# Optimization experiments

Hardware: AMD Instinct MI355X
Metric: run time of the kernel (lower is better)

## Reference

```python
import jax, jax.numpy as jnp
import numpy as np

L, B, D, H = 128, 4, 768, 300
NT, NR = 7, 12  # ner tags, relation types
EPS = 1e-5


def _cummax(v):
    # torch: cumsum(softmax(v, -1), -1)
    return jnp.cumsum(jax.nn.softmax(v, axis=-1), axis=-1)


def _layernorm(v, g, b):
    mu = jnp.mean(v, axis=-1, keepdims=True)
    var = jnp.var(v, axis=-1, keepdims=True)
    return (v - mu) * jax.lax.rsqrt(var + EPS) * g + b


def setup_inputs() -> dict:
    key = jax.random.key(0)
    ks = jax.random.split(key, 24)
    s = lambda fan_in: 1.0 / np.sqrt(fan_in)
    u = lambda k, shape, sc: jax.random.uniform(k, shape, jnp.float32, -sc, sc)
    inp = {
        "x": jax.random.normal(ks[0], (L, B, D), jnp.float32),
        "mask": jnp.ones((L, B), jnp.float32),
        # PFN_Unit
        "W_ih": u(ks[1], (5 * H, D), s(D)), "b_ih": u(ks[2], (5 * H,), s(D)),
        "W_hh": u(ks[3], (5 * H, H), s(H)), "b_hh": u(ks[4], (5 * H,), s(H)),
        "W_tr": u(ks[5], (H, 3 * H), s(3 * H)), "b_tr": u(ks[6], (H,), s(3 * H)),
        # NERUnit
        "n_W": u(ks[7], (H, 2 * H), s(2 * H)), "n_b": u(ks[8], (H,), s(2 * H)),
        "ner_hW": u(ks[9], (H, 3 * H), s(3 * H)), "ner_hb": u(ks[10], (H,), s(3 * H)),
        "ner_g": jnp.ones((H,), jnp.float32), "ner_beta": jnp.zeros((H,), jnp.float32),
        "ner_tW": u(ks[11], (NT, H), s(H)), "ner_tb": u(ks[12], (NT,), s(H)),
        # ReUnit
        "r_W": u(ks[13], (H, 2 * H), s(2 * H)), "r_b": u(ks[14], (H,), s(2 * H)),
        "re_hW": u(ks[15], (H, 3 * H), s(3 * H)), "re_hb": u(ks[16], (H,), s(3 * H)),
        "re_g": jnp.ones((H,), jnp.float32), "re_beta": jnp.zeros((H,), jnp.float32),
        "re_tW": u(ks[17], (NR, H), s(H)), "re_tb": u(ks[18], (NR,), s(H)),
    }
    return inp


def _encoder(x, W_ih, b_ih, W_hh, b_hh, W_tr, b_tr):
    pre = jnp.einsum('lbd,gd->lbg', x, W_ih) + b_ih  # precompute input transform [L,B,5H]

    def step(carry, gx):
        h, c_in = carry
        gates = gx + h @ W_hh.T + b_hh
        c, eg_cin, rg_cin, eg_c, rg_c = jnp.split(gates, 5, axis=1)
        eg_cin, rg_cin = 1.0 - _cummax(eg_cin), _cummax(rg_cin)
        eg_c, rg_c = 1.0 - _cummax(eg_c), _cummax(rg_c)
        c = jnp.tanh(c)
        ov_c = rg_c * eg_c
        up_c, dn_c = rg_c - ov_c, eg_c - ov_c
        ov_i = rg_cin * eg_cin
        up_i, dn_i = rg_cin - ov_i, eg_cin - ov_i
        share = ov_i * c_in + ov_c * c
        c_re = up_i * c_in + up_c * c + share
        c_ner = dn_i * c_in + dn_c * c + share
        c_out = jnp.concatenate([c_re, c_ner, share], axis=-1) @ W_tr.T + b_tr
        h_out = jnp.tanh(c_out)
        return (h_out, c_out), (jnp.tanh(c_ner), jnp.tanh(c_re), jnp.tanh(share))

    h0 = jnp.zeros((x.shape[1], W_hh.shape[1]), x.dtype)
    _, (h_ner, h_re, h_share) = jax.lax.scan(step, (h0, h0), pre)
    return h_ner, h_re, h_share  # each [L,B,H]


def _pair_unit(h_task, h_share, mask, gW, gb, hW, hb, ln_g, ln_b, tW, tb, diag):
    length = h_task.shape[0]
    # global feature: tanh(Linear(cat(share, task))), max over time
    h_glob = jnp.tanh(jnp.concatenate([h_share, h_task], axis=-1) @ gW.T + gb)  # [L,B,H]
    g = jnp.max(h_glob, axis=0)  # [B,H]
    # pairwise feature [L,L,B,3H] = cat(start, end, global)
    st = jnp.broadcast_to(h_task[:, None], (length, length) + h_task.shape[1:])
    en = jnp.broadcast_to(h_task[None, :], (length, length) + h_task.shape[1:])
    gb4 = jnp.broadcast_to(g, (length, length) + g.shape)
    feat = jnp.concatenate([st, en, gb4], axis=-1)
    out = _layernorm(feat @ hW.T + hb, ln_g, ln_b)
    out = jax.nn.elu(out)  # eval mode: dropout is identity
    out = jax.nn.sigmoid(out @ tW.T + tb)  # [L,L,B,T]
    # mask
    m = mask[:, None, :] * mask[None, :, :]  # [L,L,B]
    if diag:
        m = m * jnp.triu(jnp.ones((length, length), out.dtype))[:, :, None]
    return out * m[..., None]


def reference(x, mask, W_ih, b_ih, W_hh, b_hh, W_tr, b_tr,
              n_W, n_b, ner_hW, ner_hb, ner_g, ner_beta, ner_tW, ner_tb,
              r_W, r_b, re_hW, re_hb, re_g, re_beta, re_tW, re_tb):
    h_ner, h_re, h_share = _encoder(x, W_ih, b_ih, W_hh, b_hh, W_tr, b_tr)
    ner = _pair_unit(h_ner, h_share, mask, n_W, n_b, ner_hW, ner_hb,
                     ner_g, ner_beta, ner_tW, ner_tb, diag=True)
    re = _pair_unit(h_re, h_share, mask, r_W, r_b, re_hW, re_hb,
                    re_g, re_beta, re_tW, re_tb, diag=False)
    return ner, re
```

## Files before the change

### kernel.cpp

```cpp
#include <hip/hip_runtime.h>

#define LLEN 128
#define BB 4
#define DD 768
#define HH 300
#define G5 1500
#define H3 900
#define NTT 7
#define NRR 12
#define NCHB 10
#define RPB 150
#define OPB 30

#define C_WIH  0
#define C_X    1152000
#define C_WHH2 1545216
#define C_WTR2 1995216
#define F_BIH  2265216
#define F_BTR  2266720
#define F_PRE  2267040
#define F_HG0  (F_PRE)
#define F_HG1  (F_PRE+153600)
#define F_A0   (F_PRE+307200)
#define F_E0   (F_PRE+460800)
#define F_GF0  (F_PRE+616832)
#define F_GF1  (F_PRE+618048)
#define F_HNER (F_PRE+768000)
#define F_HRE  (F_HNER+153600)
#define F_HSH  (F_HRE+153600)
#define F_A1   0
#define F_E1   153600
#define F_AUX  (F_HSH+153600)
#define AUXB   2432
#define AUX_FL 9728
#define WS_NEED_BYTES ((size_t)(F_AUX+11776)*4)

typedef unsigned short u16;
typedef unsigned int u32;
typedef float f4 __attribute__((ext_vector_type(4)));

__device__ __forceinline__ float bf2f(u16 u) {
  union { u32 i; float f; } v; v.i = ((u32)u) << 16; return v.f;
}
__device__ __forceinline__ u16 f2bf(float f) {
  union { float f; u32 i; } v; v.f = f;
  u32 r = v.i + 0x7fffu + ((v.i >> 16) & 1u);
  return (u16)(r >> 16);
}
__device__ __forceinline__ float ldin(const void* p, int i, bool f32) {
  return f32 ? ((const float*)p)[i] : bf2f(((const u16*)p)[i]);
}
__device__ __forceinline__ bool is32(const void* mk) {
  return ((const u16*)mk)[0] == 0;
}
__device__ __forceinline__ float wsum(float x) {
  #pragma unroll
  for (int d = 1; d < 64; d <<= 1) x += __shfl_xor(x, d);
  return x;
}
__device__ __forceinline__ float aload(const float* p) {
  int v = __hip_atomic_load((const int*)p, __ATOMIC_RELAXED, __HIP_MEMORY_SCOPE_AGENT);
  union { int i; float f; } u; u.i = v; return u.f;
}
__device__ __forceinline__ void astore(float* p, float v) {
  union { float f; int i; } u; u.f = v;
  __hip_atomic_store((int*)p, u.i, __ATOMIC_RELAXED, __HIP_MEMORY_SCOPE_AGENT);
}
__device__ __forceinline__ void gbar(int* flag, int tid, int target) {
  __syncthreads();
  if (tid == 0) {
    __builtin_amdgcn_s_waitcnt(0);
    __hip_atomic_fetch_add(flag, 1, __ATOMIC_RELAXED, __HIP_MEMORY_SCOPE_AGENT);
    while (__hip_atomic_load(flag, __ATOMIC_RELAXED, __HIP_MEMORY_SCOPE_AGENT) < target)
      __builtin_amdgcn_s_sleep(1);
  }
  __syncthreads();
}

__device__ __forceinline__ f4 ld4_l2(const f4* p) {
  f4 v;
  asm volatile("global_load_dwordx4 %0, %1, off sc0\n\ts_waitcnt vmcnt(0)"
               : "=v"(v) : "v"(p) : "memory");
  return v;
}
__device__ __forceinline__ float ld1_l2(const float* p) {
  float v;
  asm volatile("global_load_dword %0, %1, off sc0\n\ts_waitcnt vmcnt(0)"
               : "=v"(v) : "v"(p) : "memory");
  return v;
}
__device__ __forceinline__ int ldi_l2(const int* p) {
  int v;
  asm volatile("global_load_dword %0, %1, off sc0\n\ts_waitcnt vmcnt(0)"
               : "=v"(v) : "v"(p) : "memory");
  return v;
}
__device__ __forceinline__ void gbarL2(int* flag, int tid, int target) {
  __builtin_amdgcn_s_waitcnt(0);
  __syncthreads();
  if (tid == 0) {
    __builtin_amdgcn_s_waitcnt(0);
    __hip_atomic_fetch_add(flag, 1, __ATOMIC_RELAXED, __HIP_MEMORY_SCOPE_WORKGROUP);
    int it = 0;
    while (ldi_l2(flag) < target) {
      __builtin_amdgcn_s_sleep(1);
      if (++it > 100000) break;
    }
  }
  __syncthreads();
}
__device__ __forceinline__ void exst(float* p, float v, int mode) {
  if (mode) *p = v; else astore(p, v);
}

__global__ void k_canon(const void* xo, const void* mk, const void* Wih, const void* bih,
                        const void* Whh, const void* bhh, const void* Wtr, const void* btr,
                        float* ws) {
  bool f32 = is32(mk);
  int piece = blockIdx.y;
  int i = blockIdx.x * 256 + threadIdx.x;
  switch (piece) {
    case 0: if (!f32 && i < 1152000) ws[C_WIH + i] = ldin(Wih, i, f32); break;
    case 1: if (!f32 && i < 393216)  ws[C_X + i]   = ldin(xo, i, f32);  break;
    case 2: if (i < 225000) {
      int k2 = i / G5, out = i - k2 * G5;
      float2 v;
      v.x = ldin(Whh, out * HH + 2 * k2, f32);
      v.y = ldin(Whh, out * HH + 2 * k2 + 1, f32);
      ((float2*)(ws + C_WHH2))[i] = v;
    } break;
    case 3: if (i < 135000) {
      int k2 = i / HH, out = i - k2 * HH;
      float2 v;
      v.x = ldin(Wtr, out * H3 + 2 * k2, f32);
      v.y = ldin(Wtr, out * H3 + 2 * k2 + 1, f32);
      ((float2*)(ws + C_WTR2))[i] = v;
    } break;
    case 4: {
      if (i < 1504) ws[F_BIH + i] = (i < G5) ? ldin(bih, i, f32) + ldin(bhh, i, f32) : 0.f;
      else if (i < 1824) { int j = i - 1504; ws[F_BTR + j] = (j < HH) ? ldin(btr, j, f32) : 0.f; }
    } break;
    case 5: if (i < 11776) ws[F_AUX + i] = 0.f; break;
  }
}

__global__ void k_pre2(const void* xo, const void* Wo, const void* mk,
                       const float* cX, const float* cW, const float* biasf, float* pre) {
  bool f32 = is32(mk);
  const float* X = f32 ? (const float*)xo : cX;
  const float* W = f32 ? (const float*)Wo : cW;
  __shared__ __align__(16) float xl[8 * DD];
  int tid = threadIdx.x;
  int lb0 = (blockIdx.x >> 1) * 8;
  int half = blockIdx.x & 1;
  for (int e = tid; e < 8 * DD; e += 256) xl[e] = X[(size_t)lb0 * DD + e];
  __syncthreads();
  for (int j = half * 750 + tid; j < half * 750 + 750; j += 256) {
    const float4* w = (const float4*)(W + (size_t)j * DD);
    float acc[8] = {0.f, 0.f, 0.f, 0.f, 0.f, 0.f, 0.f, 0.f};
    #pragma unroll 2
    for (int k = 0; k < DD / 4; ++k) {
      float4 u = w[k];
      #pragma unroll
      for (int r = 0; r < 8; ++r) {
        const float4 p = *(const float4*)(xl + r * DD + k * 4);
        acc[r] += u.x * p.x + u.y * p.y + u.z * p.z + u.w * p.w;
      }
    }
    float bias = biasf[j];
    #pragma unroll
    for (int r = 0; r < 8; ++r) pre[(size_t)(lb0 + r) * G5 + j] = acc[r] + bias;
  }
}

__global__ void __launch_bounds__(512, 2) k_scan6(const float* pre, const float2* W2h, const float2* W2t,
                                                  const float* btrf, float* hner, float* hre, float* hsh,
                                                  float* aux) {
  __shared__ __align__(16) float h_l[304];
  __shared__ __align__(16) float ci_l[304];
  __shared__ __align__(16) float ga_l[1504];
  __shared__ __align__(16) float cat_l[904];
  __shared__ __align__(16) float ps[512];
  __shared__ __align__(16) float sums_l[8];
  __shared__ float exv[160];
  __shared__ float pp[40];
  __shared__ int s_bc;
  __shared__ int s_mode;
  int tid = threadIdx.x;
  int* ibase = (int*)(aux + AUX_FL);
  if (tid == 0) {
    int* cl = ibase + 1024;
    unsigned xcd;
    asm volatile("s_getreg_b32 %0, hwreg(HW_REG_XCC_ID)" : "=s"(xcd));
    xcd &= 7u;
    int rank = __hip_atomic_fetch_add(cl + xcd, 1, __ATOMIC_RELAXED, __HIP_MEMORY_SCOPE_AGENT);
    __hip_atomic_fetch_add(cl + 8, 1, __ATOMIC_RELAXED, __HIP_MEMORY_SCOPE_AGENT);
    int it = 0;
    while (__hip_atomic_load(cl + 8, __ATOMIC_RELAXED, __HIP_MEMORY_SCOPE_AGENT) < (int)gridDim.x) {
      __builtin_amdgcn_s_sleep(2);
      if (++it > 200000) break;
    }
    int base = 0;
    for (unsigned x = 0; x < xcd; ++x)
      base += __hip_atomic_load(cl + x, __ATOMIC_RELAXED, __HIP_MEMORY_SCOPE_AGENT) / NCHB;
    int cnt = __hip_atomic_load(cl + xcd, __ATOMIC_RELAXED, __HIP_MEMORY_SCOPE_AGENT);
    int slot = base + rank / NCHB;
    s_bc = (rank < (cnt / NCHB) * NCHB && slot < BB) ? (slot * 16 + rank % NCHB) : -1;
  }
  __syncthreads();
  int bc = s_bc;
  if (bc < 0) return;
  int b = bc >> 4, ch = bc & 15;
  int s = ch >> 1;
  int r0 = ch * RPB;
  float* gb   = aux + b * AUXB;
  float* cb   = gb + 1504;
  float* hb   = gb + 1808;
  float* sums = gb + 2112;
  int* flags = ibase + b * 256;

  {
    int* atf = ibase + 1088 + b * 32;
    float* tst = gb + 2176;
    int* seflag = (int*)(gb + 2208);
    if (ch == 0 && tid == 0) tst[0] = 1.0f;
    gbar(atf + 0, tid, NCHB);
    if (tid == 0) { float w1 = ld1_l2(tst); (void)w1; }
    gbar(atf + 1, tid, NCHB);
    if (ch == 0 && tid == 0) {
      tst[0] = 2.0f;
      __builtin_amdgcn_s_waitcnt(0);
    }
    if (ch == 1 && tid == 0)
      __hip_atomic_fetch_add(seflag, 1, __ATOMIC_RELAXED, __HIP_MEMORY_SCOPE_WORKGROUP);
    gbar(atf + 2, tid, NCHB);
    if (tid == 0) {
      float w2 = ld1_l2(tst);
      int fv = ldi_l2(seflag);
      if (w2 != 2.0f || fv != 1)
        __hip_atomic_fetch_or(atf + 4, 1, __ATOMIC_RELAXED, __HIP_MEMORY_SCOPE_AGENT);
    }
    gbar(atf + 3, tid, NCHB);
    if (tid == 0)
      s_mode = (__hip_atomic_load(atf + 4, __ATOMIC_RELAXED, __HIP_MEMORY_SCOPE_AGENT) == 0) ? 1 : 0;
    __syncthreads();
  }
  int mode = s_mode;

  for (int i = tid; i < 304; i += 512) { h_l[i] = 0.f; ci_l[i] = 0.f; }
  int j = tid / RPB, r = tid - j * RPB;
  int o2 = tid % OPB, jj = tid / OPB;
  int kb = j * 100;

  float2 wh[50];
  if (tid < 450) {
    const float2* wp = W2h + (size_t)(j * 50) * G5 + (r0 + r);
    #pragma unroll
    for (int kk = 0; kk < 50; ++kk) wh[kk] = wp[(size_t)kk * G5];
  }
  float2 wt[29];
  int k2b = jj * 29;
  int k2e = (k2b + 29 < 450) ? (k2b + 29) : 450;
  int nk2 = k2e - k2b;
  if (tid < 480) {
    const float2* wp = W2t + (size_t)k2b * HH + (ch * OPB + o2);
    #pragma unroll
    for (int q = 0; q < 29; ++q) if (q < nk2) wt[q] = wp[(size_t)q * HH];
  }
  __syncthreads();

  for (int t = 0; t < LLEN; ++t) {
    float pv = 0.f;
    if (j == 0 && tid < 450) pv = pre[((size_t)t * BB + b) * G5 + r0 + r];
    if (t > 0) {
      if (mode) {
        if (tid < 75)       { f4 v = ld4_l2((const f4*)hb + tid); *(f4*)(h_l + 4 * tid) = v; }
        else if (tid < 150) { int q = tid - 75; f4 v = ld4_l2((const f4*)cb + q); *(f4*)(ci_l + 4 * q) = v; }
      } else {
        for (int i = tid; i < HH; i += 512) { h_l[i] = aload(hb + i); ci_l[i] = aload(cb + i); }
      }
      __syncthreads();
    }
    if (tid < 450) {
      float acc = pv;
      if (t > 0) {
        #pragma unroll
        for (int kk = 0; kk < 50; ++kk)
          acc += wh[kk].x * h_l[kb + 2 * kk] + wh[kk].y * h_l[kb + 2 * kk + 1];
      }
      ps[tid] = acc;
    }
    __syncthreads();
    if (tid < RPB) {
      float g = ps[tid] + ps[RPB + tid] + ps[2 * RPB + tid];
      if (s == 0) exst(gb + r0 + tid, tanhf(g), mode);
      else exv[tid] = __expf(g);
    }
    __syncthreads();
    if (s > 0) {
      if (tid < 30) {
        int base2 = tid * 5;
        pp[tid] = ((exv[base2] + exv[base2+1]) + (exv[base2+2] + exv[base2+3])) + exv[base2+4];
      }
      __syncthreads();
      if (tid == 0) {
        float run = 0.f;
        for (int i = 0; i < 30; ++i) { float tv = pp[i]; pp[i] = run; run += tv; }
        exst(sums + (ch - 2), run, mode);
      }
      __syncthreads();
      if (tid < 30) {
        int base2 = tid * 5;
        float run = pp[tid];
        run += exv[base2];     exst(gb + r0 + base2,     run, mode);
        run += exv[base2 + 1]; exst(gb + r0 + base2 + 1, run, mode);
        run += exv[base2 + 2]; exst(gb + r0 + base2 + 2, run, mode);
        run += exv[base2 + 3]; exst(gb + r0 + base2 + 3, run, mode);
        run += exv[base2 + 4]; exst(gb + r0 + base2 + 4, run, mode);
      }
    }
    if (mode) gbarL2(flags + 2 * t, tid, NCHB); else gbar(flags + 2 * t, tid, NCHB);
    if (mode) {
      if (tid < 375)      { f4 v = ld4_l2((const f4*)gb + tid); *(f4*)(ga_l + 4 * tid) = v; }
      else if (tid < 377) { int q = tid - 375; f4 v = ld4_l2((const f4*)sums + q); *(f4*)(sums_l + 4 * q) = v; }
    } else {
      for (int i = tid; i < G5; i += 512) ga_l[i] = aload(gb + i);
      if (tid < 8) sums_l[tid] = aload(sums + tid);
    }
    __syncthreads();
    if (tid < HH) {
      float c = ga_l[tid];
      float v[4];
      #pragma unroll
      for (int s1 = 0; s1 < 4; ++s1) {
        float raw = ga_l[(s1 + 1) * HH + tid];
        float off = (tid >= RPB) ? sums_l[2 * s1] : 0.f;
        float S = sums_l[2 * s1] + sums_l[2 * s1 + 1];
        v[s1] = (raw + off) / S;
      }
      float eg_cin = 1.f - v[0], rg_cin = v[1], eg_c = 1.f - v[2], rg_c = v[3];
      float ci = (t > 0) ? ci_l[tid] : 0.f;
      float ov_c = rg_c * eg_c;
      float up_c = rg_c - ov_c, dn_c = eg_c - ov_c;
      float ov_i = rg_cin * eg_cin;
      float up_i = rg_cin - ov_i, dn_i = eg_cin - ov_i;
      float share = ov_i * ci + ov_c * c;
      float c_re  = up_i * ci + up_c * c + share;
      float c_ner = dn_i * ci + dn_c * c + share;
      cat_l[tid] = c_re; cat_l[HH + tid] = c_ner; cat_l[2 * HH + tid] = share;
      int sb = ch * OPB;
      if (tid >= sb && tid < sb + OPB) {
        size_t ob = ((size_t)t * BB + b) * HH + tid;
        hner[ob] = tanhf(c_ner); hre[ob] = tanhf(c_re); hsh[ob] = tanhf(share);
      }
    }
    __syncthreads();
    if (tid < 480) {
      float acc = 0.f;
      #pragma unroll
      for (int q = 0; q < 29; ++q)
        if (q < nk2) acc += wt[q].x * cat_l[2 * (k2b + q)] + wt[q].y * cat_l[2 * (k2b + q) + 1];
      ps[tid] = acc;
    }
    __syncthreads();
    if (tid < OPB) {
      float co = btrf[ch * OPB + tid];
      #pragma unroll
      for (int q = 0; q < 16; ++q) co += ps[q * OPB + tid];
      exst(cb + ch * OPB + tid, co, mode);
      exst(hb + ch * OPB + tid, tanhf(co), mode);
    }
    if (mode) gbarL2(flags + 2 * t + 1, tid, NCHB); else gbar(flags + 2 * t + 1, tid, NCHB);
  }
}

__global__ void k_glob3(const float* hsh, const float* hner, const float* hre,
                        const void* nW, const void* nb, const void* rW, const void* rb,
                        const void* mk, float* hg0, float* hg1) {
  bool f32 = is32(mk);
  int task = blockIdx.x >> 7;
  int lb0 = (blockIdx.x & 127) * 4;
  const float* tsk = task ? hre : hner;
  const void* gWo = task ? rW : nW;
  const void* gbo = task ? rb : nb;
  float* hg = task ? hg1 : hg0;
  __shared__ __align__(16) float catl[2400];
  int tid = threadIdx.x;
  for (int e = tid; e < 2400; e += 320) {
    int rr = e / 600, c = e - rr * 600;
    catl[e] = (c < HH) ? hsh[(size_t)(lb0 + rr) * HH + c] : tsk[(size_t)(lb0 + rr) * HH + (c - HH)];
  }
  __syncthreads();
  if (tid < HH) {
    float bias = ldin(gbo, tid, f32);
    float acc[4] = {bias, bias, bias, bias};
    if (f32) {
      const float4* row = (const float4*)((const float*)gWo + (size_t)tid * 600);
      #pragma unroll 2
      for (int k = 0; k < 150; ++k) {
        float4 u = row[k];
        #pragma unroll
        for (int rr = 0; rr < 4; ++rr) {
          const float4 cv = *(const float4*)(catl + rr * 600 + 4 * k);
          acc[rr] += u.x * cv.x + u.y * cv.y + u.z * cv.z + u.w * cv.w;
        }
      }
    } else {
      for (int k = 0; k < 600; ++k) {
        float w = ldin(gWo, tid * 600 + k, f32);
        #pragma unroll
        for (int rr = 0; rr < 4; ++rr) acc[rr] += w * catl[rr * 600 + k];
      }
    }
    #pragma unroll
    for (int rr = 0; rr < 4; ++rr) hg[(size_t)(lb0 + rr) * HH + tid] = tanhf(acc[rr]);
  }
}

__global__ void k_feat2(const float* hner, const float* hre,
                        const void* nhW, const void* nhb, const void* rhW, const void* rhb,
                        const void* mk, float* A0, float* E0, float* A1, float* E1) {
  bool f32 = is32(mk);
  int task = blockIdx.x >> 7;
  int lb0 = (blockIdx.x & 127) * 4;
  const float* tsk = task ? hre : hner;
  const void* hWo = task ? rhW : nhW;
  const void* hbo = task ? rhb : nhb;
  float* A = task ? A1 : A0;
  float* E = task ? E1 : E0;
  __shared__ __align__(16) float tl[1200];
  int tid = threadIdx.x;
  for (int e = tid; e < 1200; e += 320) {
    int rr = e / 300, c = e - rr * 300;
    tl[e] = tsk[(size_t)(lb0 + rr) * HH + c];
  }
  __syncthreads();
  if (tid < HH) {
    float bias = ldin(hbo, tid, f32);
    float a[4] = {bias, bias, bias, bias};
    float ev[4] = {0.f, 0.f, 0.f, 0.f};
    if (f32) {
      const float4* r1 = (const float4*)((const float*)hWo + (size_t)tid * H3);
      const float4* r2 = (const float4*)((const float*)hWo + (size_t)tid * H3 + HH);
      #pragma unroll 2
      for (int k = 0; k < 75; ++k) {
        float4 u = r1[k], w2 = r2[k];
        #pragma unroll
        for (int rr = 0; rr < 4; ++rr) {
          const float4 tv = *(const float4*)(tl + rr * 300 + 4 * k);
          a[rr]  += u.x * tv.x + u.y * tv.y + u.z * tv.z + u.w * tv.w;
          ev[rr] += w2.x * tv.x + w2.y * tv.y + w2.z * tv.z + w2.w * tv.w;
        }
      }
    } else {
      for (int k = 0; k < HH; ++k) {
        float w1 = ldin(hWo, tid * H3 + k, f32);
        float w2 = ldin(hWo, tid * H3 + HH + k, f32);
        #pragma unroll
        for (int rr = 0; rr < 4; ++rr) {
          a[rr] += w1 * tl[rr * 300 + k];
          ev[rr] += w2 * tl[rr * 300 + k];
        }
      }
    }
    #pragma unroll
    for (int rr = 0; rr < 4; ++rr) {
      A[(size_t)(lb0 + rr) * HH + tid] = a[rr];
      E[(size_t)(lb0 + rr) * HH + tid] = ev[rr];
    }
  }
}

__global__ void k_gmf(const float* hg0, const float* hg1, const void* nhW, const void* rhW,
                      const void* mk, float* Gf0, float* Gf1) {
  bool f32 = is32(mk);
  int task = blockIdx.x >> 2, b = blockIdx.x & 3;
  const float* hg = task ? hg1 : hg0;
  const void* hWo = task ? rhW : nhW;
  float* Gf = task ? Gf1 : Gf0;
  __shared__ __align__(16) float gl[304];
  int tid = threadIdx.x;
  if (tid < HH) {
    float m = -1e30f;
    for (int l = 0; l < LLEN; ++l) m = fmaxf(m, hg[((size_t)l * BB + b) * HH + tid]);
    gl[tid] = m;
  }
  __syncthreads();
  if (tid < HH) {
    float acc = 0.f;
    if (f32) {
      const float4* row = (const float4*)((const float*)hWo + (size_t)tid * H3 + 600);
      #pragma unroll 5
      for (int k = 0; k < 75; ++k) {
        float4 u = row[k];
        const float4 gv = *(const float4*)(gl + 4 * k);
        acc += u.x * gv.x + u.y * gv.y + u.z * gv.z + u.w * gv.w;
      }
    } else {
      for (int k = 0; k < HH; ++k) acc += gl[k] * ldin(hWo, tid * H3 + 600 + k, f32);
    }
    Gf[b * HH + tid] = acc;
  }
}

__global__ void __launch_bounds__(256) k_pair6(const float* A0, const float* E0, const float* Gf0,
                                               const void* lg0, const void* lb0_, const void* tW0, const void* tb0,
                                               const float* A1, const float* E1, const float* Gf1,
                                               const void* lg1, const void* lb1_, const void* tW1, const void* tb1,
                                               const void* mk, void* outv) {
  __shared__ float lg_l[304], lb_l[304], tb_l[16];
  __shared__ float tw_l[3616];
  bool f32 = is32(mk);
  int tau = blockIdx.x >> 12;
  int bid = blockIdx.x & 4095;
  const float* A  = tau ? A1 : A0;
  const float* E  = tau ? E1 : E0;
  const float* Gf = tau ? Gf1 : Gf0;
  const void* lgo = tau ? lg1 : lg0;
  const void* lbo = tau ? lb1_ : lb0_;
  const void* tWo = tau ? tW1 : tW0;
  const void* tbo = tau ? tb1 : tb0;
  int T = tau ? NRR : NTT;
  int diag = tau ? 0 : 1;
  int Toff = tau ? 458752 : 0;
  int tid = threadIdx.x;
  for (int i2 = tid; i2 < HH; i2 += 256) { lg_l[i2] = ldin(lgo, i2, f32); lb_l[i2] = ldin(lbo, i2, f32); }
  for (int i2 = tid; i2 < T * HH; i2 += 256) tw_l[i2] = ldin(tWo, i2, f32);
  if (tid < T) tb_l[tid] = ldin(tbo, tid, f32);
  __syncthreads();
  int i = bid >> 5;
  int j0 = (bid & 31) << 2;
  int b = tid >> 6, ln = tid & 63;
  const float* ar = A  + (size_t)(i * BB + b) * HH;
  const float* gr = Gf + (size_t)b * HH;
  bool ok4 = ln < 44;
  float a0 = ar[ln]       + gr[ln];
  float a1 = ar[64 + ln]  + gr[64 + ln];
  float a2 = ar[128 + ln] + gr[128 + ln];
  float a3 = ar[192 + ln] + gr[192 + ln];
  float a4 = ok4 ? (ar[256 + ln] + gr[256 + ln]) : 0.f;
  float mi = ldin(mk, i * BB + b, f32);
  for (int dj = 0; dj < 4; ++dj) {
    int jx = j0 + dj;
    const float* er = E + (size_t)(jx * BB + b) * HH;
    float u0 = a0 + er[ln];
    float u1 = a1 + er[64 + ln];
    float u2 = a2 + er[128 + ln];
    float u3 = a3 + er[192 + ln];
    float u4 = ok4 ? (a4 + er[256 + ln]) : 0.f;
    float s1 = ((u0 + u1) + (u2 + u3)) + u4;
    float s2 = ((u0 * u0 + u1 * u1) + (u2 * u2 + u3 * u3)) + u4 * u4;
    #pragma unroll
    for (int d = 1; d < 64; d <<= 1) { s1 += __shfl_xor(s1, d); s2 += __shfl_xor(s2, d); }
    float mean = s1 * (1.f / 300.f);
    float var = s2 * (1.f / 300.f) - mean * mean;
    float rstd = rsqrtf(var + 1e-5f);
    {
      float y;
      y = (u0 - mean) * rstd * lg_l[ln]       + lb_l[ln];       u0 = (y > 0.f) ? y : __expf(y) - 1.f;
      y = (u1 - mean) * rstd * lg_l[64 + ln]  + lb_l[64 + ln];  u1 = (y > 0.f) ? y : __expf(y) - 1.f;
      y = (u2 - mean) * rstd * lg_l[128 + ln] + lb_l[128 + ln]; u2 = (y > 0.f) ? y : __expf(y) - 1.f;
      y = (u3 - mean) * rstd * lg_l[192 + ln] + lb_l[192 + ln]; u3 = (y > 0.f) ? y : __expf(y) - 1.f;
      if (ok4) {
        y = (u4 - mean) * rstd * lg_l[256 + ln] + lb_l[256 + ln];
        u4 = (y > 0.f) ? y : __expf(y) - 1.f;
      }
    }
    float m = mi * ldin(mk, jx * BB + b, f32);
    if (diag && jx < i) m = 0.f;
    size_t obase = (size_t)Toff + ((size_t)(i * LLEN + jx) * BB + b) * T;
    float mine = 0.f;
    for (int t = 0; t < T; ++t) {
      const float* twr = tw_l + t * HH;
      float s = u0 * twr[ln] + u1 * twr[64 + ln] + u2 * twr[128 + ln] + u3 * twr[192 + ln];
      if (ok4) s += u4 * twr[256 + ln];
      s = wsum(s);
      s += tb_l[t];
      float o = m / (1.f + __expf(-s));
      mine = (ln == t) ? o : mine;
    }
    if (ln < T) {
      if (f32) ((float*)outv)[obase + ln] = mine;
      else ((u16*)outv)[obase + ln] = f2bf(mine);
    }
  }
}

__global__ void k_sent(const void* mk, const void* xo, void* outv, int hostcode) {
  __shared__ int bad;
  if (threadIdx.x == 0) bad = 0;
  __syncthreads();
  bool f32 = is32(mk);
  for (int i = threadIdx.x; i < 4096; i += 256) {
    float v = ldin(xo, i, f32);
    if (!(v == v) || fabsf(v) > 1e6f) bad = 1;
  }
  __syncthreads();
  if (threadIdx.x == 0) {
    float code = (float)hostcode;
    if (bad) code = fmaxf(code, 88.f);
    if (code > 0.f) {
      if (f32) ((float*)outv)[0] = code;
      else ((u16*)outv)[0] = f2bf(code);
    }
  }
}

extern "C" void kernel_launch(void* const* d_in, const int* in_sizes, int n_in,
                              void* d_out, int out_size, void* d_ws, size_t ws_size,
                              hipStream_t stream) {
  const void* x    = d_in[0];
  const void* mask = d_in[1];
  const void* Wih  = d_in[2];
  const void* bih  = d_in[3];
  const void* Whh  = d_in[4];
  const void* bhh  = d_in[5];
  const void* Wtr  = d_in[6];
  const void* btr  = d_in[7];
  const void* nW   = d_in[8];
  const void* nb   = d_in[9];
  const void* nhW  = d_in[10];
  const void* nhb  = d_in[11];
  const void* ng   = d_in[12];
  const void* nbe  = d_in[13];
  const void* ntW  = d_in[14];
  const void* ntb  = d_in[15];
  const void* rW   = d_in[16];
  const void* rb   = d_in[17];
  const void* rhW  = d_in[18];
  const void* rhb  = d_in[19];
  const void* rg   = d_in[20];
  const void* rbe  = d_in[21];
  const void* rtW  = d_in[22];
  const void* rtb  = d_in[23];
  float* ws = (float*)d_ws;

  static const int exp_sz[24] = {393216, 512, 1152000, 1500, 450000, 1500, 270000, 300,
                                 180000, 300, 270000, 300, 300, 300, 2100, 7,
                                 180000, 300, 270000, 300, 300, 300, 3600, 12};
  int hostcode = 0;
  if (n_in != 24) hostcode = 890;
  else {
    for (int ii = 0; ii < 24; ++ii)
      if (in_sizes[ii] != exp_sz[ii]) { hostcode = 900 + ii; break; }
  }
  if (hostcode == 0 && out_size != 1245184) hostcode = 880;
  if (hostcode == 0 && ws_size < WS_NEED_BYTES) hostcode = 1099;

  dim3 gc(4500, 6);
  k_canon<<<gc, 256, 0, stream>>>(x, mask, Wih, bih, Whh, bhh, Wtr, btr, ws);
  k_pre2<<<128, 256, 0, stream>>>(x, Wih, mask, ws + C_X, ws + C_WIH, ws + F_BIH, ws + F_PRE);
  k_scan6<<<256, 512, 0, stream>>>(ws + F_PRE, (const float2*)(ws + C_WHH2), (const float2*)(ws + C_WTR2),
                                   ws + F_BTR, ws + F_HNER, ws + F_HRE, ws + F_HSH, ws + F_AUX);
  k_glob3<<<256, 320, 0, stream>>>(ws + F_HSH, ws + F_HNER, ws + F_HRE,
                                   nW, nb, rW, rb, mask, ws + F_HG0, ws + F_HG1);
  k_feat2<<<256, 320, 0, stream>>>(ws + F_HNER, ws + F_HRE, nhW, nhb, rhW, rhb, mask,
                                   ws + F_A0, ws + F_E0, ws + F_A1, ws + F_E1);
  k_gmf<<<8, 320, 0, stream>>>(ws + F_HG0, ws + F_HG1, nhW, rhW, mask, ws + F_GF0, ws + F_GF1);
  k_pair6<<<8192, 256, 0, stream>>>(ws + F_A0, ws + F_E0, ws + F_GF0, ng, nbe, ntW, ntb,
                                    ws + F_A1, ws + F_E1, ws + F_GF1, rg, rbe, rtW, rtb,
                                    mask, d_out);
  k_sent<<<1, 256, 0, stream>>>(mask, x, d_out, hostcode);
}
```

Before: 1.527 ms.

## Replace counter barriers with per-chunk slot barriers and prefetch next-step inputs

The recurrent scan kernel's per-step grid barriers, which used an atomic counter per step, are replaced by per-chunk token slots. Each block writes its own slot and 64 threads poll all ten slots with vector loads that bypass the cache. The softmax-cumsum prefix over 30 partial sums becomes a wavefront shuffle scan instead of a serial single-thread loop, which removes two block syncs. The next step's precomputed input is prefetched during the barrier wait, and the final barrier is skipped. Spin timeouts are shortened, which risks silent desync if a block stalls longer than the limit.

```diff
diff --git a/kernel.cpp b/kernel.cpp
--- a/kernel.cpp
+++ b/kernel.cpp
@@ -38,6 +38,7 @@
 typedef unsigned short u16;
 typedef unsigned int u32;
 typedef float f4 __attribute__((ext_vector_type(4)));
+typedef int i4 __attribute__((ext_vector_type(4)));
 
 __device__ __forceinline__ float bf2f(u16 u) {
   union { u32 i; float f; } v; v.i = ((u32)u) << 16; return v.f;
@@ -58,10 +59,6 @@
   for (int d = 1; d < 64; d <<= 1) x += __shfl_xor(x, d);
   return x;
 }
-__device__ __forceinline__ float aload(const float* p) {
-  int v = __hip_atomic_load((const int*)p, __ATOMIC_RELAXED, __HIP_MEMORY_SCOPE_AGENT);
-  union { int i; float f; } u; u.i = v; return u.f;
-}
 __device__ __forceinline__ void astore(float* p, float v) {
   union { float f; int i; } u; u.f = v;
   __hip_atomic_store((int*)p, u.i, __ATOMIC_RELAXED, __HIP_MEMORY_SCOPE_AGENT);
@@ -71,46 +68,100 @@
   if (tid == 0) {
     __builtin_amdgcn_s_waitcnt(0);
     __hip_atomic_fetch_add(flag, 1, __ATOMIC_RELAXED, __HIP_MEMORY_SCOPE_AGENT);
-    while (__hip_atomic_load(flag, __ATOMIC_RELAXED, __HIP_MEMORY_SCOPE_AGENT) < target)
+    int it = 0;
+    while (__hip_atomic_load(flag, __ATOMIC_RELAXED, __HIP_MEMORY_SCOPE_AGENT) < target) {
       __builtin_amdgcn_s_sleep(1);
-  }
-  __syncthreads();
-}
-
-__device__ __forceinline__ f4 ld4_l2(const f4* p) {
+      if (++it > 50000) break;
+    }
+  }
+  __syncthreads();
+}
+__device__ __forceinline__ f4 ld4x(const f4* p, int mode) {
   f4 v;
-  asm volatile("global_load_dwordx4 %0, %1, off sc0\n\ts_waitcnt vmcnt(0)"
-               : "=v"(v) : "v"(p) : "memory");
+  if (mode)
+    asm volatile("global_load_dwordx4 %0, %1, off sc0\n\ts_waitcnt vmcnt(0)"
+                 : "=v"(v) : "v"(p) : "memory");
+  else
+    asm volatile("global_load_dwordx4 %0, %1, off sc0 sc1\n\ts_waitcnt vmcnt(0)"
+                 : "=v"(v) : "v"(p) : "memory");
   return v;
 }
-__device__ __forceinline__ float ld1_l2(const float* p) {
+__device__ __forceinline__ float ld1x(const float* p, int mode) {
   float v;
-  asm volatile("global_load_dword %0, %1, off sc0\n\ts_waitcnt vmcnt(0)"
-               : "=v"(v) : "v"(p) : "memory");
+  if (mode)
+    asm volatile("global_load_dword %0, %1, off sc0\n\ts_waitcnt vmcnt(0)"
+                 : "=v"(v) : "v"(p) : "memory");
+  else
+    asm volatile("global_load_dword %0, %1, off sc0 sc1\n\ts_waitcnt vmcnt(0)"
+                 : "=v"(v) : "v"(p) : "memory");
   return v;
 }
-__device__ __forceinline__ int ldi_l2(const int* p) {
+__device__ __forceinline__ int ldix(const int* p, int mode) {
   int v;
-  asm volatile("global_load_dword %0, %1, off sc0\n\ts_waitcnt vmcnt(0)"
-               : "=v"(v) : "v"(p) : "memory");
+  if (mode)
+    asm volatile("global_load_dword %0, %1, off sc0\n\ts_waitcnt vmcnt(0)"
+                 : "=v"(v) : "v"(p) : "memory");
+  else
+    asm volatile("global_load_dword %0, %1, off sc0 sc1\n\ts_waitcnt vmcnt(0)"
+                 : "=v"(v) : "v"(p) : "memory");
   return v;
-}
-__device__ __forceinline__ void gbarL2(int* flag, int tid, int target) {
-  __builtin_amdgcn_s_waitcnt(0);
-  __syncthreads();
-  if (tid == 0) {
-    __builtin_amdgcn_s_waitcnt(0);
-    __hip_atomic_fetch_add(flag, 1, __ATOMIC_RELAXED, __HIP_MEMORY_SCOPE_WORKGROUP);
-    int it = 0;
-    while (ldi_l2(flag) < target) {
-      __builtin_amdgcn_s_sleep(1);
-      if (++it > 100000) break;
-    }
-  }
-  __syncthreads();
 }
 __device__ __forceinline__ void exst(float* p, float v, int mode) {
   if (mode) *p = v; else astore(p, v);
+}
+__device__ __forceinline__ int poll10(const int* slots, int tok, int mode) {
+  i4 a, b, c;
+  if (mode)
+    asm volatile("global_load_dwordx4 %0, %3, off sc0\n\t"
+                 "global_load_dwordx4 %1, %4, off sc0\n\t"
+                 "global_load_dwordx4 %2, %5, off sc0\n\t"
+                 "s_waitcnt vmcnt(0)"
+                 : "=&v"(a), "=&v"(b), "=&v"(c)
+                 : "v"(slots), "v"(slots + 4), "v"(slots + 8) : "memory");
+  else
+    asm volatile("global_load_dwordx4 %0, %3, off sc0 sc1\n\t"
+                 "global_load_dwordx4 %1, %4, off sc0 sc1\n\t"
+                 "global_load_dwordx4 %2, %5, off sc0 sc1\n\t"
+                 "s_waitcnt vmcnt(0)"
+                 : "=&v"(a), "=&v"(b), "=&v"(c)
+                 : "v"(slots), "v"(slots + 4), "v"(slots + 8) : "memory");
+  return (a.x >= tok) & (a.y >= tok) & (a.z >= tok) & (a.w >= tok) &
+         (b.x >= tok) & (b.y >= tok) & (b.z >= tok) & (b.w >= tok) &
+         (c.x >= tok) & (c.y >= tok);
+}
+__device__ __forceinline__ void sbar(int* slots, int ch, int tok, int tid, int mode) {
+  asm volatile("s_waitcnt vmcnt(0)" ::: "memory");
+  __syncthreads();
+  if (tid == 0) {
+    if (mode) slots[ch] = tok;
+    else __hip_atomic_store(slots + ch, tok, __ATOMIC_RELAXED, __HIP_MEMORY_SCOPE_AGENT);
+  }
+  if (tid < 64) {
+    int it = 0;
+    while (!poll10(slots, tok, mode)) {
+      __builtin_amdgcn_s_sleep(1);
+      if (++it > 5000) break;
+    }
+  }
+  __syncthreads();
+}
+__device__ __forceinline__ int claim_bc(int* cl, int nb) {
+  unsigned xcd;
+  asm volatile("s_getreg_b32 %0, hwreg(HW_REG_XCC_ID)" : "=s"(xcd));
+  xcd &= 7u;
+  int rank = __hip_atomic_fetch_add(cl + xcd, 1, __ATOMIC_RELAXED, __HIP_MEMORY_SCOPE_AGENT);
+  __hip_atomic_fetch_add(cl + 8, 1, __ATOMIC_RELAXED, __HIP_MEMORY_SCOPE_AGENT);
+  int it = 0;
+  while (__hip_atomic_load(cl + 8, __ATOMIC_RELAXED, __HIP_MEMORY_SCOPE_AGENT) < nb) {
+    __builtin_amdgcn_s_sleep(2);
+    if (++it > 100000) break;
+  }
+  int base = 0;
+  for (unsigned x = 0; x < xcd; ++x)
+    base += __hip_atomic_load(cl + x, __ATOMIC_RELAXED, __HIP_MEMORY_SCOPE_AGENT) / NCHB;
+  int cnt = __hip_atomic_load(cl + xcd, __ATOMIC_RELAXED, __HIP_MEMORY_SCOPE_AGENT);
+  int slot = base + rank / NCHB;
+  return (rank < (cnt / NCHB) * NCHB && slot < BB) ? (slot * 16 + rank % NCHB) : -1;
 }
 
 __global__ void k_canon(const void* xo, const void* mk, const void* Wih, const void* bih,
@@ -173,7 +224,7 @@
   }
 }
 
-__global__ void __launch_bounds__(512, 2) k_scan6(const float* pre, const float2* W2h, const float2* W2t,
+__global__ void __launch_bounds__(512, 2) k_scan8(const float* pre, const float2* W2h, const float2* W2t,
                                                   const float* btrf, float* hner, float* hre, float* hsh,
                                                   float* aux) {
   __shared__ __align__(16) float h_l[304];
@@ -183,30 +234,10 @@
   __shared__ __align__(16) float ps[512];
   __shared__ __align__(16) float sums_l[8];
   __shared__ float exv[160];
-  __shared__ float pp[40];
-  __shared__ int s_bc;
-  __shared__ int s_mode;
+  __shared__ int s_bc, s_mode;
   int tid = threadIdx.x;
   int* ibase = (int*)(aux + AUX_FL);
-  if (tid == 0) {
-    int* cl = ibase + 1024;
-    unsigned xcd;
-    asm volatile("s_getreg_b32 %0, hwreg(HW_REG_XCC_ID)" : "=s"(xcd));
-    xcd &= 7u;
-    int rank = __hip_atomic_fetch_add(cl + xcd, 1, __ATOMIC_RELAXED, __HIP_MEMORY_SCOPE_AGENT);
-    __hip_atomic_fetch_add(cl + 8, 1, __ATOMIC_RELAXED, __HIP_MEMORY_SCOPE_AGENT);
-    int it = 0;
-    while (__hip_atomic_load(cl + 8, __ATOMIC_RELAXED, __HIP_MEMORY_SCOPE_AGENT) < (int)gridDim.x) {
-      __builtin_amdgcn_s_sleep(2);
-      if (++it > 200000) break;
-    }
-    int base = 0;
-    for (unsigned x = 0; x < xcd; ++x)
-      base += __hip_atomic_load(cl + x, __ATOMIC_RELAXED, __HIP_MEMORY_SCOPE_AGENT) / NCHB;
-    int cnt = __hip_atomic_load(cl + xcd, __ATOMIC_RELAXED, __HIP_MEMORY_SCOPE_AGENT);
-    int slot = base + rank / NCHB;
-    s_bc = (rank < (cnt / NCHB) * NCHB && slot < BB) ? (slot * 16 + rank % NCHB) : -1;
-  }
+  if (tid == 0) s_bc = claim_bc(ibase, (int)gridDim.x);
   __syncthreads();
   int bc = s_bc;
   if (bc < 0) return;
@@ -217,26 +248,24 @@
   float* cb   = gb + 1504;
   float* hb   = gb + 1808;
   float* sums = gb + 2112;
-  int* flags = ibase + b * 256;
+  int* slotsA = ibase + 32 + b * 64;
+  int* slotsB = slotsA + 16;
+  int* atf    = slotsA + 32;
 
   {
-    int* atf = ibase + 1088 + b * 32;
     float* tst = gb + 2176;
     int* seflag = (int*)(gb + 2208);
     if (ch == 0 && tid == 0) tst[0] = 1.0f;
     gbar(atf + 0, tid, NCHB);
-    if (tid == 0) { float w1 = ld1_l2(tst); (void)w1; }
+    if (tid == 0) { float w1 = ld1x(tst, 1); (void)w1; }
     gbar(atf + 1, tid, NCHB);
-    if (ch == 0 && tid == 0) {
-      tst[0] = 2.0f;
-      __builtin_amdgcn_s_waitcnt(0);
-    }
+    if (ch == 0 && tid == 0) { tst[0] = 2.0f; __builtin_amdgcn_s_waitcnt(0); }
     if (ch == 1 && tid == 0)
       __hip_atomic_fetch_add(seflag, 1, __ATOMIC_RELAXED, __HIP_MEMORY_SCOPE_WORKGROUP);
     gbar(atf + 2, tid, NCHB);
     if (tid == 0) {
-      float w2 = ld1_l2(tst);
-      int fv = ldi_l2(seflag);
+      float w2 = ld1x(tst, 1);
+      int fv = ldix(seflag, 1);
       if (w2 != 2.0f || fv != 1)
         __hip_atomic_fetch_or(atf + 4, 1, __ATOMIC_RELAXED, __HIP_MEMORY_SCOPE_AGENT);
     }
@@ -247,7 +276,6 @@
   }
   int mode = s_mode;
 
-  for (int i = tid; i < 304; i += 512) { h_l[i] = 0.f; ci_l[i] = 0.f; }
   int j = tid / RPB, r = tid - j * RPB;
   int o2 = tid % OPB, jj = tid / OPB;
   int kb = j * 100;
@@ -267,22 +295,18 @@
     #pragma unroll
     for (int q = 0; q < 29; ++q) if (q < nk2) wt[q] = wp[(size_t)q * HH];
   }
+  float pv = 0.f;
+  if (tid < RPB) pv = pre[(size_t)b * G5 + r0 + tid];
   __syncthreads();
 
   for (int t = 0; t < LLEN; ++t) {
-    float pv = 0.f;
-    if (j == 0 && tid < 450) pv = pre[((size_t)t * BB + b) * G5 + r0 + r];
     if (t > 0) {
-      if (mode) {
-        if (tid < 75)       { f4 v = ld4_l2((const f4*)hb + tid); *(f4*)(h_l + 4 * tid) = v; }
-        else if (tid < 150) { int q = tid - 75; f4 v = ld4_l2((const f4*)cb + q); *(f4*)(ci_l + 4 * q) = v; }
-      } else {
-        for (int i = tid; i < HH; i += 512) { h_l[i] = aload(hb + i); ci_l[i] = aload(cb + i); }
-      }
+      if (tid < 75)       { f4 v = ld4x((const f4*)hb + tid, mode); *(f4*)(h_l + 4 * tid) = v; }
+      else if (tid < 150) { int q = tid - 75; f4 v = ld4x((const f4*)cb + q, mode); *(f4*)(ci_l + 4 * q) = v; }
       __syncthreads();
     }
     if (tid < 450) {
-      float acc = pv;
+      float acc = (j == 0) ? pv : 0.f;
       if (t > 0) {
         #pragma unroll
         for (int kk = 0; kk < 50; ++kk)
@@ -296,37 +320,31 @@
       if (s == 0) exst(gb + r0 + tid, tanhf(g), mode);
       else exv[tid] = __expf(g);
     }
-    __syncthreads();
     if (s > 0) {
-      if (tid < 30) {
-        int base2 = tid * 5;
-        pp[tid] = ((exv[base2] + exv[base2+1]) + (exv[base2+2] + exv[base2+3])) + exv[base2+4];
-      }
-      __syncthreads();
-      if (tid == 0) {
-        float run = 0.f;
-        for (int i = 0; i < 30; ++i) { float tv = pp[i]; pp[i] = run; run += tv; }
-        exst(sums + (ch - 2), run, mode);
-      }
       __syncthreads();
       if (tid < 30) {
         int base2 = tid * 5;
-        float run = pp[tid];
-        run += exv[base2];     exst(gb + r0 + base2,     run, mode);
-        run += exv[base2 + 1]; exst(gb + r0 + base2 + 1, run, mode);
-        run += exv[base2 + 2]; exst(gb + r0 + base2 + 2, run, mode);
-        run += exv[base2 + 3]; exst(gb + r0 + base2 + 3, run, mode);
-        run += exv[base2 + 4]; exst(gb + r0 + base2 + 4, run, mode);
-      }
-    }
-    if (mode) gbarL2(flags + 2 * t, tid, NCHB); else gbar(flags + 2 * t, tid, NCHB);
-    if (mode) {
-      if (tid < 375)      { f4 v = ld4_l2((const f4*)gb + tid); *(f4*)(ga_l + 4 * tid) = v; }
-      else if (tid < 377) { int q = tid - 375; f4 v = ld4_l2((const f4*)sums + q); *(f4*)(sums_l + 4 * q) = v; }
-    } else {
-      for (int i = tid; i < G5; i += 512) ga_l[i] = aload(gb + i);
-      if (tid < 8) sums_l[tid] = aload(sums + tid);
-    }
+        float e0 = exv[base2], e1 = exv[base2 + 1], e2 = exv[base2 + 2],
+              e3 = exv[base2 + 3], e4 = exv[base2 + 4];
+        float p = ((e0 + e1) + (e2 + e3)) + e4;
+        float inc = p;
+        #pragma unroll
+        for (int d = 1; d < 32; d <<= 1) { float o = __shfl_up(inc, d); if (tid >= d) inc += o; }
+        float tot = __shfl(inc, 29);
+        float run = inc - p;
+        run += e0; exst(gb + r0 + base2,     run, mode);
+        run += e1; exst(gb + r0 + base2 + 1, run, mode);
+        run += e2; exst(gb + r0 + base2 + 2, run, mode);
+        run += e3; exst(gb + r0 + base2 + 3, run, mode);
+        run += e4; exst(gb + r0 + base2 + 4, run, mode);
+        if (tid == 0) exst(sums + (ch - 2), tot, mode);
+      }
+    }
+    sbar(slotsA, ch, t + 1, tid, mode);
+    if (tid < 375)      { f4 v = ld4x((const f4*)gb + tid, mode); *(f4*)(ga_l + 4 * tid) = v; }
+    else if (tid < 377) { int q = tid - 375; f4 v = ld4x((const f4*)sums + q, mode); *(f4*)(sums_l + 4 * q) = v; }
+    float pvn = 0.f;
+    if (t + 1 < LLEN && tid < RPB) pvn = pre[((size_t)(t + 1) * BB + b) * G5 + r0 + tid];
     __syncthreads();
     if (tid < HH) {
       float c = ga_l[tid];
@@ -370,7 +388,8 @@
       exst(cb + ch * OPB + tid, co, mode);
       exst(hb + ch * OPB + tid, tanhf(co), mode);
     }
-    if (mode) gbarL2(flags + 2 * t + 1, tid, NCHB); else gbar(flags + 2 * t + 1, tid, NCHB);
+    if (t + 1 < LLEN) sbar(slotsB, ch, t + 1, tid, mode);
+    pv = pvn;
   }
 }
 
@@ -650,7 +669,7 @@
   dim3 gc(4500, 6);
   k_canon<<<gc, 256, 0, stream>>>(x, mask, Wih, bih, Whh, bhh, Wtr, btr, ws);
   k_pre2<<<128, 256, 0, stream>>>(x, Wih, mask, ws + C_X, ws + C_WIH, ws + F_BIH, ws + F_PRE);
-  k_scan6<<<256, 512, 0, stream>>>(ws + F_PRE, (const float2*)(ws + C_WHH2), (const float2*)(ws + C_WTR2),
+  k_scan8<<<256, 512, 0, stream>>>(ws + F_PRE, (const float2*)(ws + C_WHH2), (const float2*)(ws + C_WTR2),
                                    ws + F_BTR, ws + F_HNER, ws + F_HRE, ws + F_HSH, ws + F_AUX);
   k_glob3<<<256, 320, 0, stream>>>(ws + F_HSH, ws + F_HNER, ws + F_HRE,
                                    nW, nb, rW, rb, mask, ws + F_HG0, ws + F_HG1);
```

After: 1.471 ms. -3.7%, faster.
